# Kernel tuning notes

Measured on AMD Instinct MI355X. Metric: run time of the kernel, lower is better.

Reference implementation:

```python
import jax, jax.numpy as jnp
import numpy as np

B, C, H, W = 4, 256, 64, 64


def _radius_bias(h, w):
    # Attention_Radius: grid coords (x: 1..W, y: H..1), pairwise euclidean dist
    y = jnp.arange(h, 0, -1, dtype=jnp.float32)
    x = jnp.arange(1, w + 1, dtype=jnp.float32)
    yy, xx = jnp.meshgrid(y, x, indexing='ij')
    coords = jnp.stack([xx.reshape(-1), yy.reshape(-1)], axis=1)  # [N,2]
    diff = coords[:, None, :] - coords[None, :, :]                # [N,N,2]
    dist = jnp.sqrt(jnp.sum(diff * diff, axis=-1))                # [N,N]
    # Weight_Mapping: linearly map to [0.5,2] with inversion (far -> small)
    lo, hi = jnp.float32(0.5), jnp.float32(2.0)
    return hi - (dist - dist.min()) * (hi - lo) / (dist.max() - dist.min())


def setup_inputs() -> dict:
    key = jax.random.key(0)
    k1, k2, k3, k4 = jax.random.split(key, 4)
    scale = 1.0 / np.sqrt(C)
    return {
        'x': jax.random.normal(k1, (B, C, H, W), dtype=jnp.float32),
        'w_phi': jax.random.normal(k2, (C, C), dtype=jnp.float32) * scale,
        'w_theta': jax.random.normal(k3, (C, C), dtype=jnp.float32) * scale,
        'w_g': jax.random.normal(k4, (C, C), dtype=jnp.float32) * scale,
    }


def reference(x, w_phi, w_theta, w_g):
    b, c, h, w = x.shape
    n = h * w
    xf = x.reshape(b, c, n)                                  # [b,c,N]
    phi = jnp.einsum('dc,bcn->bdn', w_phi, xf)               # [b,c,N]
    theta = jnp.einsum('dc,bcn->bnd', w_theta, xf)           # [b,N,c]
    g = jnp.einsum('dc,bcn->bnd', w_g, xf)                   # [b,N,c]
    scores = jnp.einsum('bnc,bcm->bnm', theta, phi)          # [b,N,N]
    scores = _radius_bias(h, w) * scores                     # multiplicative radius bias
    attn = jax.nn.softmax(scores, axis=1)                    # NOTE: softmax over dim=1 (rows)
    out = jnp.einsum('bnm,bmc->bnc', attn, g)                # [b,N,c]
    out = out.transpose(0, 2, 1).reshape(b, c, h, w)
    return out + x
```

## Files before the change

### kernel.cpp

```cpp
#include <hip/hip_runtime.h>
#include <math.h>

typedef unsigned short ush;
typedef short short8 __attribute__((ext_vector_type(8)));
typedef int i32x4 __attribute__((ext_vector_type(4)));
typedef int i32x16 __attribute__((ext_vector_type(16)));
typedef float f32x16 __attribute__((ext_vector_type(16)));
typedef unsigned int u32;

namespace {
constexpr int B = 4, C = 256, N = 4096, NCH = 4;
constexpr size_t PL8 = (size_t)B * N * C;
constexpr size_t OFF_TH  = 0;
constexpr size_t OFF_TL  = PL8;
constexpr size_t OFF_PH  = 2 * PL8;
constexpr size_t OFF_PLO = 3 * PL8;
constexpr size_t OFF_G   = 4 * PL8;
constexpr size_t FOFF    = 4 * PL8 + (size_t)B * C * N * 2;
constexpr size_t F_PM = 0;
constexpr size_t F_PS = (size_t)B * NCH * N;

constexpr size_t OFF_XH = 26ull * 1024 * 1024;
constexpr size_t OFF_XL = OFF_XH + (size_t)B * N * C * 2;
constexpr size_t OFF_WH = OFF_XL + (size_t)B * N * C * 2;
constexpr size_t OFF_WL = OFF_WH + (size_t)3 * C * C * 2;
constexpr size_t WS_NEED = OFF_WL + (size_t)3 * C * C * 2;

constexpr float SCL = 8.0f / 127.0f;
constexpr float S2  = SCL * SCL;
constexpr float RB  = 1.5f / 89.09545f;
constexpr float L2E = 1.44269504f;
constexpr float BA2  = 2.0f * S2 * L2E;
constexpr float BBC2 = RB * S2 * L2E;
constexpr float C1  = 1.0f / 254.0f;
constexpr float INV_SCL = 127.0f / 8.0f;
}

#define MFMAI8(a, b, c)  __builtin_amdgcn_mfma_i32_32x32x32_i8((a), (b), (c), 0, 0, 0)
#define MFMABF(a, b, c)  __builtin_amdgcn_mfma_f32_32x32x16_bf16((a), (b), (c), 0, 0, 0)

#define WAITV(n) asm volatile("s_waitcnt vmcnt(" #n ")" ::: "memory")
#define WAITVL(n) asm volatile("s_waitcnt vmcnt(" #n ") lgkmcnt(0)" ::: "memory")
#define PBAR __builtin_amdgcn_s_barrier()

__device__ __forceinline__ float fast_exp2(float x) {
#if __has_builtin(__builtin_amdgcn_exp2f)
  return __builtin_amdgcn_exp2f(x);
#else
  float r; asm("v_exp_f32 %0, %1" : "=v"(r) : "v"(x)); return r;
#endif
}
__device__ __forceinline__ float fast_sqrt(float x) {
#if __has_builtin(__builtin_amdgcn_sqrtf)
  return __builtin_amdgcn_sqrtf(x);
#else
  float r; asm("v_sqrt_f32 %0, %1" : "=v"(r) : "v"(x)); return r;
#endif
}

__device__ __forceinline__ ush f2bf(float v) {
  u32 x = __float_as_uint(v);
  return (ush)((x + 0x7FFFu + ((x >> 16) & 1u)) >> 16);
}
__device__ __forceinline__ float bf2f(ush h) {
  return __uint_as_float(((u32)h) << 16);
}

__device__ __forceinline__ float score_i(int hh, int xx, int d2i) {
  float u = fmaf((float)xx, C1, (float)hh);
  float d = fast_sqrt((float)d2i);
  return fmaf(d, -BBC2, BA2) * u;
}

__device__ __forceinline__ void gload16(const void* g, void* l) {
  __builtin_amdgcn_global_load_lds(
      (const __attribute__((address_space(1))) u32*)(g),
      (__attribute__((address_space(3))) u32*)(l), 16, 0, 0);
}


__global__ __launch_bounds__(256) void proj_kernel(
    const float* __restrict__ x, const float* __restrict__ w_phi,
    const float* __restrict__ w_theta, const float* __restrict__ w_g,
    char* __restrict__ wsu8) {
  __shared__ float Wst[16][68];
  __shared__ float Xs[16][68];
  const int tid = threadIdx.x, tx = tid & 15, ty = tid >> 4;
  const int b = blockIdx.y / 3, p = blockIdx.y % 3;
  const int c0 = (blockIdx.x >> 6) * 64;
  const int nb = (blockIdx.x & 63) * 64;
  const float* w = (p == 0) ? w_theta : (p == 1) ? w_phi : w_g;

  float acc[4][4] = {};
  for (int kk = 0; kk < C; kk += 16) {
    {
      int r = tid >> 2, kq = (tid & 3) << 2;
      float4 v = *reinterpret_cast<const float4*>(&w[(size_t)(c0 + r) * C + kk + kq]);
      Wst[kq + 0][r] = v.x; Wst[kq + 1][r] = v.y;
      Wst[kq + 2][r] = v.z; Wst[kq + 3][r] = v.w;
    }
    {
      int k = tid >> 4, j4 = (tid & 15) << 2;
      *reinterpret_cast<float4*>(&Xs[k][j4]) =
          *reinterpret_cast<const float4*>(&x[((size_t)b * C + kk + k) * N + nb + j4]);
    }
    __syncthreads();
#pragma unroll
    for (int k2 = 0; k2 < 16; ++k2) {
      float4 av = *reinterpret_cast<const float4*>(&Wst[k2][ty << 2]);
      float4 bv = *reinterpret_cast<const float4*>(&Xs[k2][tx << 2]);
      float aa[4] = {av.x, av.y, av.z, av.w};
      float bb[4] = {bv.x, bv.y, bv.z, bv.w};
#pragma unroll
      for (int i = 0; i < 4; ++i)
#pragma unroll
        for (int j = 0; j < 4; ++j) acc[i][j] = fmaf(aa[i], bb[j], acc[i][j]);
    }
    __syncthreads();
  }

  if (p < 2) {
    char* hi = wsu8 + (p == 0 ? OFF_TH : OFF_PH) + (size_t)b * N * C;
    char* lo = wsu8 + (p == 0 ? OFF_TL : OFF_PLO) + (size_t)b * N * C;
    const int k0 = c0 + (ty << 2);
    const size_t koff = (size_t)(k0 >> 5) * 1024 + ((k0 >> 4) & 1) * 512 + (k0 & 15);
#pragma unroll
    for (int j = 0; j < 4; ++j) {
      int n = nb + (tx << 2) + j;
      u32 ph = 0, pl = 0;
#pragma unroll
      for (int i = 0; i < 4; ++i) {
        float t = acc[i][j] * INV_SCL;
        int h = __float2int_rn(t);
        h = max(-127, min(127, h));
        int l = __float2int_rn((t - (float)h) * 254.0f);
        l = max(-127, min(127, l));
        ph |= ((u32)(h & 0xFF)) << (8 * i);
        pl |= ((u32)(l & 0xFF)) << (8 * i);
      }
      size_t a = (size_t)(n >> 5) * 8192 + (size_t)(n & 31) * 16 + koff;
      *(u32*)(hi + a) = ph;
      *(u32*)(lo + a) = pl;
    }
  } else {
    ush* gp = (ush*)(wsu8 + OFF_G) + (size_t)b * C * N;
#pragma unroll
    for (int i = 0; i < 4; ++i) {
      ushort4 pk;
      pk.x = f2bf(acc[i][0]); pk.y = f2bf(acc[i][1]);
      pk.z = f2bf(acc[i][2]); pk.w = f2bf(acc[i][3]);
      *reinterpret_cast<ushort4*>(&gp[(size_t)(c0 + (ty << 2) + i) * N + nb + (tx << 2)]) = pk;
    }
  }
}

__global__ __launch_bounds__(256) void split_x(
    const float* __restrict__ x, char* __restrict__ wsu8) {
  __shared__ float Ls[64 * 66];
  const int tid = threadIdx.x;
  const int n0 = blockIdx.x * 64, c0 = blockIdx.y * 64, b = blockIdx.z;
  const float* xb = x + ((size_t)b * C + c0) * N + n0;
#pragma unroll
  for (int i = 0; i < 4; ++i) {
    int fi = i * 256 + tid, cc = fi >> 4, c4 = fi & 15;
    float4 v = *reinterpret_cast<const float4*>(xb + (size_t)cc * N + c4 * 4);
    Ls[cc * 66 + c4 * 4 + 0] = v.x; Ls[cc * 66 + c4 * 4 + 1] = v.y;
    Ls[cc * 66 + c4 * 4 + 2] = v.z; Ls[cc * 66 + c4 * 4 + 3] = v.w;
  }
  __syncthreads();
  ush* XH = (ush*)(wsu8 + OFF_XH) + ((size_t)b * N + n0) * C + c0;
  ush* XL = (ush*)(wsu8 + OFF_XL) + ((size_t)b * N + n0) * C + c0;
#pragma unroll
  for (int i = 0; i < 4; ++i) {
    int oi = i * 256 + tid, n = oi >> 4, c4 = oi & 15;
    ushort4 hv, lv;
#pragma unroll
    for (int j = 0; j < 4; ++j) {
      float v = Ls[(c4 * 4 + j) * 66 + n];
      ush h = f2bf(v);
      ush l = f2bf(v - bf2f(h));
      (&hv.x)[j] = h; (&lv.x)[j] = l;
    }
    *reinterpret_cast<ushort4*>(XH + (size_t)n * C + c4 * 4) = hv;
    *reinterpret_cast<ushort4*>(XL + (size_t)n * C + c4 * 4) = lv;
  }
}

__global__ __launch_bounds__(256) void split_w(
    const float* __restrict__ w_phi, const float* __restrict__ w_theta,
    const float* __restrict__ w_g, char* __restrict__ wsu8) {
  int id = blockIdx.x * 256 + threadIdx.x;
  int p = id / 16384, e4 = id % 16384;
  const float* w = (p == 0) ? w_theta : (p == 1) ? w_phi : w_g;
  float4 v = *reinterpret_cast<const float4*>(w + (size_t)e4 * 4);
  ush* WH = (ush*)(wsu8 + OFF_WH) + (size_t)p * C * C + (size_t)e4 * 4;
  ush* WL = (ush*)(wsu8 + OFF_WL) + (size_t)p * C * C + (size_t)e4 * 4;
  ushort4 hv, lv;
  float vv[4] = {v.x, v.y, v.z, v.w};
#pragma unroll
  for (int j = 0; j < 4; ++j) {
    ush h = f2bf(vv[j]);
    ush l = f2bf(vv[j] - bf2f(h));
    (&hv.x)[j] = h; (&lv.x)[j] = l;
  }
  *reinterpret_cast<ushort4*>(WH) = hv;
  *reinterpret_cast<ushort4*>(WL) = lv;
}

__global__ __launch_bounds__(512) void proj_mfma(char* __restrict__ wsu8) {
  __shared__ __align__(16) char plds[131072];
  const int tid = threadIdx.x, lane = tid & 63, w = tid >> 6;
  const int l31 = lane & 31, lh5 = lane >> 5;
  const int wr = w >> 2, wc = w & 3;
  const int bx = blockIdx.x;
  const int db = (bx >> 5) * 64, nb = (bx & 31) * 128;
  const int b = blockIdx.y / 3, p = blockIdx.y % 3;
  const char* xh = wsu8 + OFF_XH + (size_t)b * N * C * 2;
  const char* xl = wsu8 + OFF_XL + (size_t)b * N * C * 2;
  const char* wh = wsu8 + OFF_WH + (size_t)p * C * C * 2;
  const char* wl = wsu8 + OFF_WL + (size_t)p * C * C * 2;
  char* const Wb = plds;
  char* const Xb = plds + 65536;

#pragma unroll
  for (int cix = 0; cix < 8; ++cix) {
    int pl = cix >> 2, ci = cix & 3;
    int glin = ci * 512 + tid;
    int d = glin >> 5, g = glin & 31;
    const char* src = (pl ? wl : wh) + (size_t)(db + d) * 512 + ((g ^ (d & 15)) << 4);
    gload16(src, Wb + pl * 32768 + ci * 8192 + (tid << 4));
  }
  auto stageX = [&](int ch, int buf) {
#pragma unroll
    for (int cix = 0; cix < 4; ++cix) {
      int pl = cix >> 1, ci = cix & 1;
      int glin = ci * 512 + tid;
      int n = glin >> 3, g = glin & 7;
      const char* src = (pl ? xl : xh) +
          (size_t)(nb + n) * 512 + ch * 128 + ((g ^ (n & 7)) << 4);
      gload16(src, Xb + buf * 32768 + pl * 16384 + ci * 8192 + (tid << 4));
    }
  };
  stageX(0, 0);
  __syncthreads();

  const int arow = wr * 32 + l31;
  const int brow = wc * 32 + l31;
  f32x16 acc = {};
  for (int ch = 0; ch < 4; ++ch) {
    if (ch < 3) stageX(ch + 1, (ch + 1) & 1);
    const char* XB = Xb + (ch & 1) * 32768;
    __builtin_amdgcn_s_setprio(1);
#pragma unroll
    for (int kt = 0; kt < 4; ++kt) {
      int slw = (ch * 4 + kt) * 2 + lh5;
      int oW = ((slw ^ (arow & 15)) << 4);
      short8 wa = *(const short8*)(Wb + arow * 512 + oW);
      short8 wb2 = *(const short8*)(Wb + 32768 + arow * 512 + oW);
      int slx = kt * 2 + lh5;
      int oX = ((slx ^ (brow & 7)) << 4);
      short8 xa = *(const short8*)(XB + brow * 128 + oX);
      short8 xb2 = *(const short8*)(XB + 16384 + brow * 128 + oX);
      acc = MFMABF(wa, xa, acc);
      acc = MFMABF(wa, xb2, acc);
      acc = MFMABF(wb2, xa, acc);
    }
    __builtin_amdgcn_s_setprio(0);
    __syncthreads();
  }

  const int n = nb + wc * 32 + l31;
  if (p < 2) {
    char* hi = wsu8 + (p == 0 ? OFF_TH : OFF_PH) + (size_t)b * N * C;
    char* lo = wsu8 + (p == 0 ? OFF_TL : OFF_PLO) + (size_t)b * N * C;
#pragma unroll
    for (int q = 0; q < 4; ++q) {
      u32 phv = 0, plv = 0;
#pragma unroll
      for (int j = 0; j < 4; ++j) {
        float t = acc[q * 4 + j] * INV_SCL;
        int h = __float2int_rn(t);
        h = max(-127, min(127, h));
        int l = __float2int_rn((t - (float)h) * 254.0f);
        l = max(-127, min(127, l));
        phv |= ((u32)(h & 0xFF)) << (8 * j);
        plv |= ((u32)(l & 0xFF)) << (8 * j);
      }
      int dd = db + wr * 32 + 8 * q + 4 * lh5;
      size_t a = (size_t)(n >> 5) * 8192 + (size_t)(dd >> 5) * 1024 +
                 ((dd >> 4) & 1) * 512 + (size_t)(n & 31) * 16 + (dd & 15);
      *(u32*)(hi + a) = phv;
      *(u32*)(lo + a) = plv;
    }
  } else {
    ush* gp = (ush*)(wsu8 + OFF_G) + (size_t)b * C * N;
#pragma unroll
    for (int r = 0; r < 16; ++r) {
      int dd = db + wr * 32 + (r & 3) + 8 * (r >> 2) + 4 * lh5;
      gp[(size_t)dd * N + n] = f2bf(acc[r]);
    }
  }
}

__global__ __launch_bounds__(512, 4) void stats_kernel(
    const char* __restrict__ wsu8, float* __restrict__ fws) {
  __shared__ __align__(16) char lds[65536];
  const int tid = threadIdx.x, lane = tid & 63, w = tid >> 6;
  const int l31 = lane & 31, lh5 = lane >> 5;
  const int wr = w >> 2, wc = w & 3;
  int flat = (blockIdx.z * NCH + blockIdx.y) * 32 + blockIdx.x;
  int nf = ((flat & 7) << 6) | (flat >> 3);
  const int b = nf >> 7, rem = nf & 127, chunk = rem >> 5, mt = rem & 31;
  const int mb = mt * 128, cbase = chunk * 1024;
  const size_t bo = (size_t)b * N * C;
  const char* th  = wsu8 + OFF_TH + bo;
  const char* tl  = wsu8 + OFF_TL + bo;
  const char* ph  = wsu8 + OFF_PH + bo;
  const char* plo = wsu8 + OFF_PLO + bo;

  const int brow = wc * 32 + l31;
  i32x4 FH[8];
  {
    const char* prh = ph + (size_t)((mb >> 5) + wc) * 8192 + lh5 * 512 + l31 * 16;
#pragma unroll
    for (int q = 0; q < 8; ++q) FH[q] = *(const i32x4*)(prh + q * 1024);
  }
#pragma unroll
  for (int i = 0; i < 4; ++i)
    gload16(plo + (size_t)(mb >> 5) * 8192 + i * 8192 + tid * 16,
            lds + i * 8192 + tid * 16);
  char* const T0 = lds + 32768;
  char* const T1 = lds + 49152;

  auto stage = [&](int s, char* dst) {
    int ntx = s >> 1, h = s & 1;
    int g2 = tid >> 8;
    int inr = (tid & 255) * 16;
#pragma unroll
    for (int plane = 0; plane < 2; ++plane) {
      const char* src = (plane ? tl : th) +
          (size_t)((cbase >> 5) + ntx * 2 + g2) * 8192 + h * 4096 + inr;
      gload16(src, dst + plane * 8192 + g2 * 4096 + inr);
    }
  };
  stage(0, T0);
  __syncthreads();

  const int m = mb + brow;
  const int mcl = m & 63, mh = m >> 6;
  const int nbl = wr * 32;
  float rmax = -3e38f, rsum = 0.0f;

  u32 dxp[8];
#pragma unroll
  for (int r2 = 0; r2 < 8; ++r2) {
    int r0i = 2 * r2, r1i = 2 * r2 + 1;
    int p0 = (r0i & 3) + 8 * (r0i >> 2) + 4 * lh5;
    int p1 = (r1i & 3) + 8 * (r1i >> 2) + 4 * lh5;
    int d0 = nbl + p0 - mcl, d1 = nbl + p1 - mcl;
    dxp[r2] = (u32)(d0 * d0) | ((u32)(d1 * d1) << 16);
  }

  char* Tc = T0; char* Tn = T1;
  for (int nt = 0; nt < 16; ++nt) {
    i32x16 HH = {}, XX = {};
#pragma unroll
    for (int h = 0; h < 2; ++h) {
      int p = nt * 2 + h;
      if (p < 31) stage(p + 1, Tn);
      __builtin_amdgcn_s_setprio(1);
#pragma unroll
      for (int kt = 0; kt < 4; ++kt) {
        int g = h * 4 + kt;
        const char* aB = Tc + wr * 4096 + kt * 1024 + lh5 * 512 + l31 * 16;
        i32x4 ah = *(const i32x4*)(aB);
        i32x4 al = *(const i32x4*)(aB + 8192);
        i32x4 bl = *(const i32x4*)(lds + wc * 8192 + g * 1024 + lh5 * 512 + l31 * 16);
        HH = MFMAI8(ah, FH[g], HH);
        XX = MFMAI8(ah, bl, XX);
        XX = MFMAI8(al, FH[g], XX);
      }
      __builtin_amdgcn_s_setprio(0);
      if (h == 1) {
        int dyi = (cbase >> 6) + nt - mh;
        int dy2i = dyi * dyi;
        float bs[16];
#pragma unroll
        for (int r = 0; r < 16; ++r) {
          int d2i = (int)((dxp[r >> 1] >> ((r & 1) * 16)) & 0xFFFFu) + dy2i;
          bs[r] = score_i(HH[r], XX[r], d2i);
        }
        float m0 = fmaxf(fmaxf(fmaxf(bs[0], bs[1]), fmaxf(bs[2], bs[3])),
                         fmaxf(fmaxf(bs[4], bs[5]), fmaxf(bs[6], bs[7])));
        float m1 = fmaxf(fmaxf(fmaxf(bs[8], bs[9]), fmaxf(bs[10], bs[11])),
                         fmaxf(fmaxf(bs[12], bs[13]), fmaxf(bs[14], bs[15])));
        float nm = fmaxf(rmax, fmaxf(m0, m1));
#pragma unroll
        for (int r = 0; r < 16; ++r) bs[r] = fast_exp2(bs[r] - nm);
        float s0 = ((bs[0] + bs[1]) + (bs[2] + bs[3])) + ((bs[4] + bs[5]) + (bs[6] + bs[7]));
        float s1 = ((bs[8] + bs[9]) + (bs[10] + bs[11])) + ((bs[12] + bs[13]) + (bs[14] + bs[15]));
        rsum = fmaf(rsum, fast_exp2(rmax - nm), s0 + s1);
        rmax = nm;
      }
      __syncthreads();
      char* t = Tc; Tc = Tn; Tn = t;
    }
  }
  {
    float om = __shfl_xor(rmax, 32);
    float os = __shfl_xor(rsum, 32);
    float nm = fmaxf(rmax, om);
    rsum = rsum * fast_exp2(rmax - nm) + os * fast_exp2(om - nm);
    rmax = nm;
  }
  float* redM = (float*)lds;
  float* redS = (float*)(lds + 1024);
  if (lane < 32) {
    redM[wr * 128 + wc * 32 + l31] = rmax;
    redS[wr * 128 + wc * 32 + l31] = rsum;
  }
  __syncthreads();
  if (tid < 128) {
    float m0 = redM[tid], m1 = redM[128 + tid];
    float nm = fmaxf(m0, m1);
    float s = redS[tid] * fast_exp2(m0 - nm) + redS[128 + tid] * fast_exp2(m1 - nm);
    fws[F_PM + ((size_t)(b * NCH + chunk)) * N + mb + tid] = nm;
    fws[F_PS + ((size_t)(b * NCH + chunk)) * N + mb + tid] = s;
  }
}

__global__ __launch_bounds__(512, 1) void out_kernel(
    const float* __restrict__ x, float* __restrict__ out,
    const char* __restrict__ wsu8, const float* __restrict__ fws) {
  __shared__ __align__(16) char lds[131072];
  const int tid = threadIdx.x, lane = tid & 63, w = tid >> 6;
  const int l31 = lane & 31, lh5 = lane >> 5;
  const int wn = w >> 2, wm = w & 3;
  int flat = blockIdx.y * gridDim.x + blockIdx.x;
  int nf = ((flat & 7) << 5) | (flat >> 3);
  const int b = nf >> 6, ntile = nf & 63;
  const int n0 = ntile * 64;
  const size_t bo = (size_t)b * N * C;
  const char* th  = wsu8 + OFF_TH + bo;
  const char* tl  = wsu8 + OFF_TL + bo;
  const char* ph  = wsu8 + OFF_PH + bo;
  const char* plo = wsu8 + OFF_PLO + bo;
  const char* GPB = wsu8 + OFF_G + (size_t)b * C * N * 2;

  char* const R0 = lds;
  char* const R1 = lds + 32768;
  char* const R2 = lds + 65536;
  char* const Pb = lds + 98304;
  char* const Qb = lds + 114688;

  const int grow = w * 32 + l31;
  const int gswz = grow & 7;
  const int pcol = wm * 32 + l31;
  const int mcl = pcol & 63;

  i32x4 TH[8], TL[8];
  {
    const char* trh = th + (size_t)((n0 >> 5) + wn) * 8192 + lh5 * 512 + l31 * 16;
    const char* trl = tl + (size_t)((n0 >> 5) + wn) * 8192 + lh5 * 512 + l31 * 16;
#pragma unroll
    for (int q = 0; q < 8; ++q) {
      TH[q] = *(const i32x4*)(trh + q * 1024);
      TL[q] = *(const i32x4*)(trl + q * 1024);
    }
  }
  u32 dxp[8];
#pragma unroll
  for (int r2 = 0; r2 < 8; ++r2) {
    int r0i = 2 * r2, r1i = 2 * r2 + 1;
    int p0i = wn * 32 + (r0i & 3) + 8 * (r0i >> 2) + 4 * lh5;
    int p1i = wn * 32 + (r1i & 3) + 8 * (r1i >> 2) + 4 * lh5;
    int d0 = p0i - mcl, d1 = p1i - mcl;
    dxp[r2] = (u32)(d0 * d0) | ((u32)(d1 * d1) << 16);
  }
  {
    const float* PM = fws + F_PM + (size_t)b * NCH * N;
    const float* PS = fws + F_PS + (size_t)b * NCH * N;
    const int m8 = tid * 8;
    float4 pm[NCH][2], ps[NCH][2];
#pragma unroll
    for (int ch = 0; ch < NCH; ++ch) {
      pm[ch][0] = *reinterpret_cast<const float4*>(PM + (size_t)ch * N + m8);
      pm[ch][1] = *reinterpret_cast<const float4*>(PM + (size_t)ch * N + m8 + 4);
      ps[ch][0] = *reinterpret_cast<const float4*>(PS + (size_t)ch * N + m8);
      ps[ch][1] = *reinterpret_cast<const float4*>(PS + (size_t)ch * N + m8 + 4);
    }
    float qv[8];
#pragma unroll
    for (int j = 0; j < 8; ++j) {
      int h = j >> 2, e = j & 3;
      float M = fmaxf(fmaxf((&pm[0][h].x)[e], (&pm[1][h].x)[e]),
                      fmaxf((&pm[2][h].x)[e], (&pm[3][h].x)[e]));
      float S = 0.0f;
#pragma unroll
      for (int ch = 0; ch < NCH; ++ch)
        S += (&ps[ch][h].x)[e] * fast_exp2((&pm[ch][h].x)[e] - M);
      qv[j] = M + __log2f(S);
    }
    *reinterpret_cast<float4*>(Qb + m8 * 4) = make_float4(qv[0], qv[1], qv[2], qv[3]);
    *reinterpret_cast<float4*>(Qb + m8 * 4 + 16) = make_float4(qv[4], qv[5], qv[6], qv[7]);
  }

  auto stagePhi = [&](int m0p, int h, char* dst) {
#pragma unroll
    for (int cix = 0; cix < 4; ++cix) {
      int p2 = cix >> 1, mpair = cix & 1;
      int mb2 = mpair * 2 + (tid >> 8);
      int inr = (tid & 255) * 16;
      const char* base = p2 ? plo : ph;
      const char* src = base + (size_t)((m0p >> 5) + mb2) * 8192 + h * 4096 + inr;
      gload16(src, dst + p2 * 16384 + mb2 * 4096 + inr);
    }
  };
  auto stageG = [&](int m0g, char* dst) {
#pragma unroll
    for (int cix = 0; cix < 4; ++cix) {
      int rl = cix * 64 + w * 8 + (lane >> 3);
      int gc = lane & 7;
      const char* src = GPB + (size_t)rl * (N * 2) + (size_t)m0g * 2 + ((gc ^ (rl & 7)) << 4);
      gload16(src, dst + cix * 8192 + w * 1024 + lane * 16);
    }
  };

  stagePhi(0, 0, R0);
  stagePhi(0, 1, R1);
  WAITVL(4);
  PBAR;

  f32x16 oacc0 = {}, oacc1 = {};
  char* Bc = R0; char* Bn = R1; char* Bn2 = R2;

  for (int mc = 0; mc < 32; ++mc) {
    const int m0 = mc * 128;
    i32x16 HH = {}, XX = {};
    const int mg = m0 + pcol;
    const float Qm = *(const float*)(Qb + 4 * mg);

    stageG(m0, Bn2);
    __builtin_amdgcn_s_setprio(1);
#pragma unroll
    for (int kt = 0; kt < 4; ++kt) {
      const char* bB = Bc + wm * 4096 + kt * 1024 + lh5 * 512 + l31 * 16;
      i32x4 bh = *(const i32x4*)(bB);
      i32x4 bl = *(const i32x4*)(bB + 16384);
      HH = MFMAI8(TH[kt], bh, HH);
      XX = MFMAI8(TH[kt], bl, XX);
      XX = MFMAI8(TL[kt], bh, XX);
    }
    __builtin_amdgcn_s_setprio(0);
    WAITV(4); PBAR;

    stageG(m0 + 64, Bc);
    __builtin_amdgcn_s_setprio(1);
#pragma unroll
    for (int kt = 0; kt < 4; ++kt) {
      const char* bB = Bn + wm * 4096 + kt * 1024 + lh5 * 512 + l31 * 16;
      i32x4 bh = *(const i32x4*)(bB);
      i32x4 bl = *(const i32x4*)(bB + 16384);
      HH = MFMAI8(TH[4 + kt], bh, HH);
      XX = MFMAI8(TH[4 + kt], bl, XX);
      XX = MFMAI8(TL[4 + kt], bh, XX);
    }
    __builtin_amdgcn_s_setprio(0);
    {
      const int gP = pcol >> 3, bP = (pcol & 7) << 1;
      int dyi = ntile - (mg >> 6);
      int dy2i = dyi * dyi;
#pragma unroll
      for (int r = 0; r < 16; ++r) {
        int prow = wn * 32 + (r & 3) + 8 * (r >> 2) + 4 * lh5;
        int d2i = (int)((dxp[r >> 1] >> ((r & 1) * 16)) & 0xFFFFu) + dy2i;
        float bs = score_i(HH[r], XX[r], d2i);
        float pv = fast_exp2(bs - Qm);
        *(ush*)(Pb + prow * 256 + (((gP ^ (prow & 15)) << 4)) + bP) = f2bf(pv);
      }
    }
    WAITVL(4); PBAR;

    if (mc < 31) stagePhi(m0 + 128, 0, Bn);
    __builtin_amdgcn_s_setprio(1);
#pragma unroll
    for (int t2 = 0; t2 < 4; ++t2) {
      int gG = (((t2 * 2 + lh5) ^ gswz) << 4);
      short8 gb = *(const short8*)(Bn2 + grow * 128 + gG);
      {
        int gP0 = ((((t2 * 2 + lh5) ^ (l31 & 15)) << 4));
        short8 pa = *(const short8*)(Pb + l31 * 256 + gP0);
        oacc0 = MFMABF(pa, gb, oacc0);
      }
      {
        int ar = 32 + l31;
        int gP1 = ((((t2 * 2 + lh5) ^ (ar & 15)) << 4));
        short8 pa = *(const short8*)(Pb + ar * 256 + gP1);
        oacc1 = MFMABF(pa, gb, oacc1);
      }
    }
    __builtin_amdgcn_s_setprio(0);
    if (mc < 31) { WAITV(4); } else { WAITV(0); }
    PBAR;

    if (mc < 31) stagePhi(m0 + 128, 1, Bn2);
    __builtin_amdgcn_s_setprio(1);
#pragma unroll
    for (int t2 = 0; t2 < 4; ++t2) {
      int gG = (((t2 * 2 + lh5) ^ gswz) << 4);
      short8 gb = *(const short8*)(Bc + grow * 128 + gG);
      {
        int gP0 = ((((8 + t2 * 2 + lh5) ^ (l31 & 15)) << 4));
        short8 pa = *(const short8*)(Pb + l31 * 256 + gP0);
        oacc0 = MFMABF(pa, gb, oacc0);
      }
      {
        int ar = 32 + l31;
        int gP1 = ((((8 + t2 * 2 + lh5) ^ (ar & 15)) << 4));
        short8 pa = *(const short8*)(Pb + ar * 256 + gP1);
        oacc1 = MFMABF(pa, gb, oacc1);
      }
    }
    __builtin_amdgcn_s_setprio(0);
    if (mc < 31) { WAITV(4); } else { WAITV(0); }
    PBAR;

    char* t = Bc; Bc = Bn; Bn = Bn2; Bn2 = t;
  }

  float* Tr = (float*)lds;
  const int c = w * 32 + l31;
#pragma unroll
  for (int r = 0; r < 16; ++r) {
    int crow = (r & 3) + 8 * (r >> 2) + 4 * lh5;
    Tr[c * 65 + crow] = oacc0[r];
    Tr[c * 65 + 32 + crow] = oacc1[r];
  }
  __syncthreads();
  const float* xb = x + (size_t)b * C * N;
  float* ob = out + (size_t)b * C * N;
  for (int e = tid; e < 16384; e += 512) {
    int cc = e >> 6, nl = e & 63;
    size_t idx = (size_t)cc * N + n0 + nl;
    ob[idx] = Tr[cc * 65 + nl] + xb[idx];
  }
}

extern "C" void kernel_launch(void* const* d_in, const int* in_sizes, int n_in,
                              void* d_out, int out_size, void* d_ws, size_t ws_size,
                              hipStream_t stream) {
  const float* x       = (const float*)d_in[0];
  const float* w_phi   = (const float*)d_in[1];
  const float* w_theta = (const float*)d_in[2];
  const float* w_g     = (const float*)d_in[3];
  float* out = (float*)d_out;
  char* wsu8 = (char*)d_ws;
  float* fws = (float*)(wsu8 + FOFF);

  if (ws_size >= WS_NEED) {
    split_x<<<dim3(64, 4, 4), 256, 0, stream>>>(x, wsu8);
    split_w<<<dim3(192), 256, 0, stream>>>(w_phi, w_theta, w_g, wsu8);
    proj_mfma<<<dim3(128, 12), 512, 0, stream>>>(wsu8);
  } else {
    proj_kernel<<<dim3(256, 12), 256, 0, stream>>>(x, w_phi, w_theta, w_g, wsu8);
  }
  stats_kernel<<<dim3(32, NCH, B), 512, 0, stream>>>(wsu8, fws);
  out_kernel<<<dim3(64, B), 512, 0, stream>>>(x, out, wsu8, fws);
}
```

Before: 201.9 us.

## Load G directly into registers with MFMA-friendly layout and double-buffer phi

The G projection is now written in a tiled layout matching the bf16 MFMA B-operand fragment. The out kernel loads G straight from global memory into registers, double-buffered across iterations, instead of staging it through LDS. Phi staging becomes a full 128-column double buffer in an enlarged 160KB LDS, with plain __syncthreads replacing the hand-tuned vmcnt waits. This removes LDS traffic for G and halves the barrier count per iteration. In exchange it uses more registers and gives up the finer-grained overlap of partial waits.

```diff
diff --git a/kernel.cpp b/kernel.cpp
--- a/kernel.cpp
+++ b/kernel.cpp
@@ -38,10 +38,6 @@
 
 #define MFMAI8(a, b, c)  __builtin_amdgcn_mfma_i32_32x32x32_i8((a), (b), (c), 0, 0, 0)
 #define MFMABF(a, b, c)  __builtin_amdgcn_mfma_f32_32x32x16_bf16((a), (b), (c), 0, 0, 0)
-
-#define WAITV(n) asm volatile("s_waitcnt vmcnt(" #n ")" ::: "memory")
-#define WAITVL(n) asm volatile("s_waitcnt vmcnt(" #n ") lgkmcnt(0)" ::: "memory")
-#define PBAR __builtin_amdgcn_s_barrier()
 
 __device__ __forceinline__ float fast_exp2(float x) {
 #if __has_builtin(__builtin_amdgcn_exp2f)
@@ -143,13 +139,16 @@
       *(u32*)(lo + a) = pl;
     }
   } else {
-    ush* gp = (ush*)(wsu8 + OFF_G) + (size_t)b * C * N;
+    char* gp = wsu8 + OFF_G + (size_t)b * C * N * 2;
+    const int n4 = nb + (tx << 2);
 #pragma unroll
     for (int i = 0; i < 4; ++i) {
+      int c = c0 + (ty << 2) + i;
       ushort4 pk;
       pk.x = f2bf(acc[i][0]); pk.y = f2bf(acc[i][1]);
       pk.z = f2bf(acc[i][2]); pk.w = f2bf(acc[i][3]);
-      *reinterpret_cast<ushort4*>(&gp[(size_t)(c0 + (ty << 2) + i) * N + nb + (tx << 2)]) = pk;
+      size_t a = ((size_t)(c >> 5) * 512 + (n4 >> 3)) * 512 + (c & 31) * 16 + (n4 & 7) * 2;
+      *reinterpret_cast<ushort4*>(gp + a) = pk;
     }
   }
 }
@@ -293,11 +292,12 @@
       *(u32*)(lo + a) = plv;
     }
   } else {
-    ush* gp = (ush*)(wsu8 + OFF_G) + (size_t)b * C * N;
+    char* gp = wsu8 + OFF_G + (size_t)b * C * N * 2;
 #pragma unroll
     for (int r = 0; r < 16; ++r) {
       int dd = db + wr * 32 + (r & 3) + 8 * (r >> 2) + 4 * lh5;
-      gp[(size_t)dd * N + n] = f2bf(acc[r]);
+      size_t a = ((size_t)(dd >> 5) * 512 + (n >> 3)) * 512 + (dd & 31) * 16 + (n & 7) * 2;
+      *(ush*)(gp + a) = f2bf(acc[r]);
     }
   }
 }
@@ -432,7 +432,7 @@
 __global__ __launch_bounds__(512, 1) void out_kernel(
     const float* __restrict__ x, float* __restrict__ out,
     const char* __restrict__ wsu8, const float* __restrict__ fws) {
-  __shared__ __align__(16) char lds[131072];
+  __shared__ __align__(16) char lds[163840];
   const int tid = threadIdx.x, lane = tid & 63, w = tid >> 6;
   const int l31 = lane & 31, lh5 = lane >> 5;
   const int wn = w >> 2, wm = w & 3;
@@ -447,14 +447,9 @@
   const char* plo = wsu8 + OFF_PLO + bo;
   const char* GPB = wsu8 + OFF_G + (size_t)b * C * N * 2;
 
-  char* const R0 = lds;
-  char* const R1 = lds + 32768;
-  char* const R2 = lds + 65536;
-  char* const Pb = lds + 98304;
-  char* const Qb = lds + 114688;
-
-  const int grow = w * 32 + l31;
-  const int gswz = grow & 7;
+  char* const Pb = lds + 131072;
+  char* const Qb = lds + 147456;
+
   const int pcol = wm * 32 + l31;
   const int mcl = pcol & 63;
 
@@ -516,54 +511,41 @@
       gload16(src, dst + p2 * 16384 + mb2 * 4096 + inr);
     }
   };
-  auto stageG = [&](int m0g, char* dst) {
-#pragma unroll
-    for (int cix = 0; cix < 4; ++cix) {
-      int rl = cix * 64 + w * 8 + (lane >> 3);
-      int gc = lane & 7;
-      const char* src = GPB + (size_t)rl * (N * 2) + (size_t)m0g * 2 + ((gc ^ (rl & 7)) << 4);
-      gload16(src, dst + cix * 8192 + w * 1024 + lane * 16);
+  auto ldG = [&](int m0g, short8 (&GR)[8]) {
+    const char* base = GPB + ((size_t)(w * 512 + (m0g >> 3) + lh5)) * 512 + l31 * 16;
+#pragma unroll
+    for (int q = 0; q < 8; ++q) {
+      int off = ((q >> 2) * 8 + (q & 3) * 2) * 512;
+      GR[q] = *(const short8*)(base + off);
     }
   };
 
-  stagePhi(0, 0, R0);
-  stagePhi(0, 1, R1);
-  WAITVL(4);
-  PBAR;
+  short8 GA[8], GB[8];
+  stagePhi(0, 0, lds);
+  stagePhi(0, 1, lds + 32768);
+  ldG(0, GA);
+  __syncthreads();
 
   f32x16 oacc0 = {}, oacc1 = {};
-  char* Bc = R0; char* Bn = R1; char* Bn2 = R2;
-
-  for (int mc = 0; mc < 32; ++mc) {
+
+  auto body = [&](int mc, short8 (&GU)[8], short8 (&GP)[8]) {
+    char* const Pcur = lds + (mc & 1) * 65536;
+    char* const Pnxt = lds + ((mc + 1) & 1) * 65536;
     const int m0 = mc * 128;
-    i32x16 HH = {}, XX = {};
     const int mg = m0 + pcol;
     const float Qm = *(const float*)(Qb + 4 * mg);
-
-    stageG(m0, Bn2);
+    i32x16 HH = {}, XX = {};
+
     __builtin_amdgcn_s_setprio(1);
 #pragma unroll
-    for (int kt = 0; kt < 4; ++kt) {
-      const char* bB = Bc + wm * 4096 + kt * 1024 + lh5 * 512 + l31 * 16;
+    for (int kt = 0; kt < 8; ++kt) {
+      const char* bB = Pcur + (kt >> 2) * 32768 + wm * 4096 + (kt & 3) * 1024 +
+                       lh5 * 512 + l31 * 16;
       i32x4 bh = *(const i32x4*)(bB);
       i32x4 bl = *(const i32x4*)(bB + 16384);
       HH = MFMAI8(TH[kt], bh, HH);
       XX = MFMAI8(TH[kt], bl, XX);
       XX = MFMAI8(TL[kt], bh, XX);
-    }
-    __builtin_amdgcn_s_setprio(0);
-    WAITV(4); PBAR;
-
-    stageG(m0 + 64, Bc);
-    __builtin_amdgcn_s_setprio(1);
-#pragma unroll
-    for (int kt = 0; kt < 4; ++kt) {
-      const char* bB = Bn + wm * 4096 + kt * 1024 + lh5 * 512 + l31 * 16;
-      i32x4 bh = *(const i32x4*)(bB);
-      i32x4 bl = *(const i32x4*)(bB + 16384);
-      HH = MFMAI8(TH[4 + kt], bh, HH);
-      XX = MFMAI8(TH[4 + kt], bl, XX);
-      XX = MFMAI8(TL[4 + kt], bh, XX);
     }
     __builtin_amdgcn_s_setprio(0);
     {
@@ -579,53 +561,36 @@
         *(ush*)(Pb + prow * 256 + (((gP ^ (prow & 15)) << 4)) + bP) = f2bf(pv);
       }
     }
-    WAITVL(4); PBAR;
-
-    if (mc < 31) stagePhi(m0 + 128, 0, Bn);
+    __syncthreads();
+
+    if (mc < 31) {
+      stagePhi(m0 + 128, 0, Pnxt);
+      stagePhi(m0 + 128, 1, Pnxt + 32768);
+      ldG(m0 + 128, GP);
+    }
     __builtin_amdgcn_s_setprio(1);
 #pragma unroll
-    for (int t2 = 0; t2 < 4; ++t2) {
-      int gG = (((t2 * 2 + lh5) ^ gswz) << 4);
-      short8 gb = *(const short8*)(Bn2 + grow * 128 + gG);
+    for (int q = 0; q < 8; ++q) {
+      int ms = (q >> 2) * 8 + (q & 3) * 2 + lh5;
+      short8 gb = GU[q];
       {
-        int gP0 = ((((t2 * 2 + lh5) ^ (l31 & 15)) << 4));
-        short8 pa = *(const short8*)(Pb + l31 * 256 + gP0);
+        short8 pa = *(const short8*)(Pb + l31 * 256 + ((ms ^ (l31 & 15)) << 4));
         oacc0 = MFMABF(pa, gb, oacc0);
       }
       {
         int ar = 32 + l31;
-        int gP1 = ((((t2 * 2 + lh5) ^ (ar & 15)) << 4));
-        short8 pa = *(const short8*)(Pb + ar * 256 + gP1);
+        short8 pa = *(const short8*)(Pb + ar * 256 + ((ms ^ (ar & 15)) << 4));
         oacc1 = MFMABF(pa, gb, oacc1);
       }
     }
     __builtin_amdgcn_s_setprio(0);
-    if (mc < 31) { WAITV(4); } else { WAITV(0); }
-    PBAR;
-
-    if (mc < 31) stagePhi(m0 + 128, 1, Bn2);
-    __builtin_amdgcn_s_setprio(1);
-#pragma unroll
-    for (int t2 = 0; t2 < 4; ++t2) {
-      int gG = (((t2 * 2 + lh5) ^ gswz) << 4);
-      short8 gb = *(const short8*)(Bc + grow * 128 + gG);
-      {
-        int gP0 = ((((8 + t2 * 2 + lh5) ^ (l31 & 15)) << 4));
-        short8 pa = *(const short8*)(Pb + l31 * 256 + gP0);
-        oacc0 = MFMABF(pa, gb, oacc0);
-      }
-      {
-        int ar = 32 + l31;
-        int gP1 = ((((8 + t2 * 2 + lh5) ^ (ar & 15)) << 4));
-        short8 pa = *(const short8*)(Pb + ar * 256 + gP1);
-        oacc1 = MFMABF(pa, gb, oacc1);
-      }
-    }
-    __builtin_amdgcn_s_setprio(0);
-    if (mc < 31) { WAITV(4); } else { WAITV(0); }
-    PBAR;
-
-    char* t = Bc; Bc = Bn; Bn = Bn2; Bn2 = t;
+    __syncthreads();
+  };
+
+#pragma unroll 1
+  for (int mc2 = 0; mc2 < 16; ++mc2) {
+    body(2 * mc2, GA, GB);
+    body(2 * mc2 + 1, GB, GA);
   }
 
   float* Tr = (float*)lds;
```

Result: slower. 211.2 us (+4.6%).
